# Kernel tuning notes

Measured on AMD Instinct MI355X. Metric: run time of the kernel, lower is better.

The kernel has to match this reference:

```python
import jax, jax.numpy as jnp
import numpy as np

B, F = 1024, 784
OUT, OR_T, AND_T = 1024, 32, 16
IDX_RANGE = 1 + 2 * F  # column 0 is the constant-true column


def setup_inputs() -> dict:
    key = jax.random.key(0)
    kx, kw = jax.random.split(key)
    # Binary inputs (0/1) stored as float32; module calls x.bool() i.e. x != 0.
    x = jax.random.randint(kx, (B, F), 0, 2).astype(jnp.float32)
    # Integer gate wiring: indices into [const_true | x | ~x].
    weights = jax.random.randint(kw, (OUT, OR_T, AND_T), 0, IDX_RANGE).astype(jnp.int32)
    return {"x": x, "weights": weights}


def reference(x, weights):
    out_f, or_t, and_t = weights.shape
    b = x.shape[0]
    xb = x != 0                                            # [B, F] bool
    ones = jnp.ones((b, 1), dtype=bool)
    x_in = jnp.concatenate([ones, xb, ~xb], axis=1)        # [B, 1+2F]
    # or_padding_mask: an OR-term is active unless all its AND indices are 0
    or_mask = ~jnp.all(weights == 0, axis=-1)              # [OUT, OR_T]
    # Gather selected booleans, then AND over and_terms, OR over or_terms
    x_sel = x_in[:, weights.reshape(-1)]                   # [B, OUT*OR_T*AND_T]
    x_bin = x_sel.reshape(b, out_f, or_t, and_t)
    x_and = jnp.all(x_bin, axis=-1) & or_mask              # [B, OUT, OR_T]
    x_or = jnp.any(x_and, axis=-1)                         # [B, OUT]
    return x_or
```

## Files before the change

kernel.cpp:

```cpp
#include <hip/hip_runtime.h>
#include <stdint.h>

#define BATCH 1024
#define FEAT  784
#define OUTF  1024
#define OR_T  32
#define AND_T 16
#define NIDX  1569
#define BSTRIDE 1600
#define NGROUP  16
#define TKDIM   512

#define BITS_BYTES (NGROUP * BSTRIDE * 8)
#define WT_OFF     208896
#define WS_NEED    (WT_OFF + (size_t)TKDIM * OUTF * 4)

#define NB_PACK 448
#define NB_TR   128

typedef unsigned long long u64;
typedef __attribute__((ext_vector_type(2))) u64 u64x2;

__global__ __launch_bounds__(64) void prep(const float* __restrict__ x,
                                           const int* __restrict__ w,
                                           u64* __restrict__ bits,
                                           int* __restrict__ wt) {
    __shared__ int t2[64 * 65];
    const int b   = blockIdx.x;
    const int tid = threadIdx.x;

    if (b < NB_PACK) {
        const int g  = b / 28;
        const int fb = b % 28;
        const float4* xrow = (const float4*)(x + (size_t)(g * 64 + tid) * FEAT);
        u64* bg = bits + (size_t)g * BSTRIDE;

        #pragma unroll
        for (int i = 0; i < 7; ++i) {
            const int f4 = fb * 7 + i;
            const float4 v = xrow[f4];
            const int f = f4 * 4;
            const u64 m0 = __ballot(v.x != 0.0f);
            const u64 m1 = __ballot(v.y != 0.0f);
            const u64 m2 = __ballot(v.z != 0.0f);
            const u64 m3 = __ballot(v.w != 0.0f);
            const u64 mv = (tid == 0) ? m0 : (tid == 1) ? m1 : (tid == 2) ? m2 : m3;
            if (tid < 4) {
                bg[1 + f + tid]   = mv;
                bg[785 + f + tid] = ~mv;
            }
        }
        if (fb == 0 && tid == 0) bg[0] = ~0ull;
    } else {
        const int b2     = b - NB_PACK;
        const int o_base  = (b2 & 15) * 64;
        const int tk_base = (b2 >> 4) * 64;

        #pragma unroll
        for (int i = 0; i < 16; ++i) {
            const int idx = i * 64 + tid;
            const int r = idx >> 4;
            const int q = idx & 15;
            const int4 v = *(const int4*)(w + (size_t)(o_base + r) * TKDIM
                                            + tk_base + q * 4);
            t2[(q * 4 + 0) * 65 + r] = v.x;
            t2[(q * 4 + 1) * 65 + r] = v.y;
            t2[(q * 4 + 2) * 65 + r] = v.z;
            t2[(q * 4 + 3) * 65 + r] = v.w;
        }
        __syncthreads();
        #pragma unroll
        for (int i = 0; i < 16; ++i) {
            const int idx = i * 64 + tid;
            const int rr = idx >> 4;
            const int qq = idx & 15;
            int4 o4;
            o4.x = t2[rr * 65 + qq * 4 + 0];
            o4.y = t2[rr * 65 + qq * 4 + 1];
            o4.z = t2[rr * 65 + qq * 4 + 2];
            o4.w = t2[rr * 65 + qq * 4 + 3];
            *(int4*)(wt + (size_t)(tk_base + rr) * OUTF + o_base + qq * 4) = o4;
        }
    }
}

__global__ __launch_bounds__(1024) void eval_logic(const int* __restrict__ wt,
                                                   const u64* __restrict__ bits,
                                                   int* __restrict__ out) {
    __shared__ u64 lbits[BSTRIDE];
    __shared__ u64 red[1024];

    const int bid = blockIdx.x;
    const int xcd = bid & 7;
    const int s   = bid >> 3;
    const int ob  = xcd + 8 * (s & 1);
    const int g   = s >> 1;
    const int tid = threadIdx.x;

    const u64* bg = bits + (size_t)g * BSTRIDE;
    if (tid < BSTRIDE / 2) {
        ((u64x2*)lbits)[tid] = ((const u64x2*)bg)[tid];
    }
    __syncthreads();

    const int o_local = tid & 63;
    const int tg      = tid >> 6;
    const int o       = ob * 64 + o_local;

    u64 orv = 0;
    #pragma unroll
    for (int tt = 0; tt < 2; ++tt) {
        const int term = tg * 2 + tt;
        const int* wcol = wt + (size_t)(term * AND_T) * OUTF + o;
        u64 a = ~0ull;
        int zor = 0;
        #pragma unroll
        for (int k = 0; k < 16; ++k) {
            const int idx = wcol[(size_t)k * OUTF];
            zor |= idx;
            a &= lbits[idx];
        }
        if (zor != 0) orv |= a;
    }

    red[tid] = orv;
    __syncthreads();

    u64 full = 0;
    #pragma unroll
    for (int j = 0; j < 16; ++j) full |= red[o_local + j * 64];

    int* outg = out + (size_t)(g * 64) * OUTF + (size_t)ob * 64;
    #pragma unroll
    for (int jj = 0; jj < 4; ++jj) {
        const int j = tg * 4 + jj;
        outg[(size_t)j * OUTF + o_local] = (int)((full >> j) & 1);
    }
}

__global__ __launch_bounds__(1024) void binlayer_fused(const float* __restrict__ x,
                                                       const int* __restrict__ w,
                                                       int* __restrict__ out) {
    __shared__ u64 lbits[BSTRIDE];
    __shared__ u64 red[1024];

    const int g    = blockIdx.x;
    const int ob   = blockIdx.y;
    const int tid  = threadIdx.x;
    const int lane = tid & 63;
    const int wv   = tid >> 6;

    const int start = wv * 12 + (wv < 4 ? wv : 4);
    const int cnt   = (wv < 4) ? 13 : 12;
    const float4* xrow = (const float4*)(x + (size_t)(g * 64 + lane) * FEAT);
    for (int i = 0; i < cnt; ++i) {
        const int f4 = start + i;
        const float4 v = xrow[f4];
        const int f = f4 * 4;
        const u64 m0 = __ballot(v.x != 0.0f);
        const u64 m1 = __ballot(v.y != 0.0f);
        const u64 m2 = __ballot(v.z != 0.0f);
        const u64 m3 = __ballot(v.w != 0.0f);
        const u64 mv = (lane == 0) ? m0 : (lane == 1) ? m1 : (lane == 2) ? m2 : m3;
        if (lane < 4) {
            lbits[1 + f + lane]   = mv;
            lbits[785 + f + lane] = ~mv;
        }
    }
    if (tid == 0) lbits[0] = ~0ull;
    __syncthreads();

    const int o_local = tid & 63;
    const int tg      = tid >> 6;
    const int o       = ob * 64 + o_local;
    const int4* wq = (const int4*)(w + ((size_t)o * OR_T + tg * 2) * AND_T);

    u64 orv = 0;
    #pragma unroll
    for (int tt = 0; tt < 2; ++tt) {
        u64 a = ~0ull;
        int zor = 0;
        #pragma unroll
        for (int k = 0; k < 4; ++k) {
            const int4 wi = wq[tt * 4 + k];
            zor |= wi.x | wi.y | wi.z | wi.w;
            a &= lbits[wi.x];
            a &= lbits[wi.y];
            a &= lbits[wi.z];
            a &= lbits[wi.w];
        }
        if (zor != 0) orv |= a;
    }

    red[tid] = orv;
    __syncthreads();

    u64 full = 0;
    #pragma unroll
    for (int j = 0; j < 16; ++j) full |= red[o_local + j * 64];

    int* outg = out + (size_t)(g * 64) * OUTF + (size_t)ob * 64;
    #pragma unroll
    for (int jj = 0; jj < 4; ++jj) {
        const int j = tg * 4 + jj;
        outg[(size_t)j * OUTF + o_local] = (int)((full >> j) & 1);
    }
}

extern "C" void kernel_launch(void* const* d_in, const int* in_sizes, int n_in,
                              void* d_out, int out_size, void* d_ws, size_t ws_size,
                              hipStream_t stream) {
    const float* x = (const float*)d_in[0];
    const int*   w = (const int*)d_in[1];
    int* out = (int*)d_out;

    if (ws_size >= WS_NEED) {
        u64* bits = (u64*)d_ws;
        int* wt   = (int*)((char*)d_ws + WT_OFF);
        prep<<<NB_PACK + NB_TR, 64, 0, stream>>>(x, w, bits, wt);
        eval_logic<<<NGROUP * (OUTF / 64), 1024, 0, stream>>>(wt, bits, out);
    } else {
        binlayer_fused<<<dim3(NGROUP, OUTF / 64), 1024, 0, stream>>>(x, w, out);
    }
}
```

Baseline: 63.92 us.

## Evaluate two batch groups per block to reuse weight index loads

Each eval_logic block now loads the bit tables of two 64-row batch groups into shared memory and handles 32 outputs with one OR-term per thread. Every weight index it loads is used for lookups in both tables. The OR reduction uses a cross-half-wavefront shuffle plus a smaller padded shared-memory pass. The goal is to halve the global reads of weight indices per output bit. The cost is more shared memory per block, and the block count stays at 256.

```diff
diff --git a/kernel.cpp b/kernel.cpp
--- a/kernel.cpp
+++ b/kernel.cpp
@@ -87,54 +87,70 @@
 __global__ __launch_bounds__(1024) void eval_logic(const int* __restrict__ wt,
                                                    const u64* __restrict__ bits,
                                                    int* __restrict__ out) {
-    __shared__ u64 lbits[BSTRIDE];
-    __shared__ u64 red[1024];
+    __shared__ u64 lb[2 * BSTRIDE];
+    __shared__ u64 redA[16 * 33];
+    __shared__ u64 redB[16 * 33];
 
     const int bid = blockIdx.x;
     const int xcd = bid & 7;
     const int s   = bid >> 3;
-    const int ob  = xcd + 8 * (s & 1);
-    const int g   = s >> 1;
+    const int obc = xcd * 4 + (s & 3);
+    const int gp  = s >> 2;
     const int tid = threadIdx.x;
 
-    const u64* bg = bits + (size_t)g * BSTRIDE;
-    if (tid < BSTRIDE / 2) {
-        ((u64x2*)lbits)[tid] = ((const u64x2*)bg)[tid];
-    }
-    __syncthreads();
-
-    const int o_local = tid & 63;
-    const int tg      = tid >> 6;
-    const int o       = ob * 64 + o_local;
-
-    u64 orv = 0;
-    #pragma unroll
-    for (int tt = 0; tt < 2; ++tt) {
-        const int term = tg * 2 + tt;
-        const int* wcol = wt + (size_t)(term * AND_T) * OUTF + o;
-        u64 a = ~0ull;
-        int zor = 0;
-        #pragma unroll
-        for (int k = 0; k < 16; ++k) {
-            const int idx = wcol[(size_t)k * OUTF];
-            zor |= idx;
-            a &= lbits[idx];
-        }
-        if (zor != 0) orv |= a;
-    }
-
-    red[tid] = orv;
-    __syncthreads();
-
-    u64 full = 0;
-    #pragma unroll
-    for (int j = 0; j < 16; ++j) full |= red[o_local + j * 64];
-
-    int* outg = out + (size_t)(g * 64) * OUTF + (size_t)ob * 64;
-    #pragma unroll
-    for (int jj = 0; jj < 4; ++jj) {
-        const int j = tg * 4 + jj;
-        outg[(size_t)j * OUTF + o_local] = (int)((full >> j) & 1);
+    const u64x2* src = (const u64x2*)(bits + (size_t)(gp * 2) * BSTRIDE);
+    for (int i = tid; i < BSTRIDE; i += 1024) ((u64x2*)lb)[i] = src[i];
+    __syncthreads();
+
+    const int o_local = tid & 31;
+    const int tg      = tid >> 5;
+    const int o       = obc * 32 + o_local;
+
+    const int* wcol = wt + (size_t)(tg * AND_T) * OUTF + o;
+    u64 aA = ~0ull, aB = ~0ull;
+    int zor = 0;
+    #pragma unroll
+    for (int k = 0; k < 16; ++k) {
+        const int idx = wcol[(size_t)k * OUTF];
+        zor |= idx;
+        aA &= lb[idx];
+        aB &= lb[BSTRIDE + idx];
+    }
+    u64 vA = (zor != 0) ? aA : 0ull;
+    u64 vB = (zor != 0) ? aB : 0ull;
+
+    {
+        unsigned int lo, hi;
+        lo = __shfl_xor((unsigned int)vA, 32);
+        hi = __shfl_xor((unsigned int)(vA >> 32), 32);
+        vA |= ((u64)hi << 32) | lo;
+        lo = __shfl_xor((unsigned int)vB, 32);
+        hi = __shfl_xor((unsigned int)(vB >> 32), 32);
+        vB |= ((u64)hi << 32) | lo;
+    }
+    const int wv   = tid >> 6;
+    const int lane = tid & 63;
+    if (lane < 32) {
+        redA[wv * 33 + o_local] = vA;
+        redB[wv * 33 + o_local] = vB;
+    }
+    __syncthreads();
+
+    const int o2    = tid & 31;
+    const int rgrp  = tid >> 5;
+    const int table = rgrp >> 4;
+    const u64* plane = table ? redB : redA;
+
+    u64 v = 0;
+    #pragma unroll
+    for (int k = 0; k < 16; ++k) v |= plane[k * 33 + o2];
+
+    const int rb = (rgrp & 15) * 4;
+    const int g  = gp * 2 + table;
+    int* outp = out + (size_t)(g * 64 + rb) * OUTF + obc * 32 + o2;
+    #pragma unroll
+    for (int i = 0; i < 4; ++i) {
+        outp[(size_t)i * OUTF] = (int)((v >> (rb + i)) & 1);
     }
 }
 
@@ -218,7 +234,7 @@
         u64* bits = (u64*)d_ws;
         int* wt   = (int*)((char*)d_ws + WT_OFF);
         prep<<<NB_PACK + NB_TR, 64, 0, stream>>>(x, w, bits, wt);
-        eval_logic<<<NGROUP * (OUTF / 64), 1024, 0, stream>>>(wt, bits, out);
+        eval_logic<<<256, 1024, 0, stream>>>(wt, bits, out);
     } else {
         binlayer_fused<<<dim3(NGROUP, OUTF / 64), 1024, 0, stream>>>(x, w, out);
     }
```

Measured after the change: 65.45 us. +2.4%, slower.
